# Optimization experiments

Hardware: AMD Instinct MI355X
Metric: run time of the kernel (lower is better)

## Reference

```python
import jax, jax.numpy as jnp
import numpy as np

N = 100000      # nodes per node type
E = 500000      # edges per relation
DIN = 128
DOUT = 128
H = 8
DK = DOUT // H  # 16
SQRT_DK = float(np.sqrt(DK))


def setup_inputs() -> dict:
    key = jax.random.key(0)
    ks = jax.random.split(key, 24)
    s = 1.0 / np.sqrt(DIN)
    inp = {
        "h_a": jax.random.normal(ks[0], (N, DIN), jnp.float32),
        "h_b": jax.random.normal(ks[1], (N, DIN), jnp.float32),
        "src0": jax.random.randint(ks[2], (E,), 0, N, jnp.int32),
        "dst0": jax.random.randint(ks[3], (E,), 0, N, jnp.int32),
        "src1": jax.random.randint(ks[4], (E,), 0, N, jnp.int32),
        "dst1": jax.random.randint(ks[5], (E,), 0, N, jnp.int32),
        "src2": jax.random.randint(ks[6], (E,), 0, N, jnp.int32),
        "dst2": jax.random.randint(ks[7], (E,), 0, N, jnp.int32),
        "Wk": jax.random.normal(ks[8], (2, DIN, DOUT), jnp.float32) * s,
        "bk": jnp.zeros((2, DOUT), jnp.float32),
        "Wv": jax.random.normal(ks[9], (2, DIN, DOUT), jnp.float32) * s,
        "bv": jnp.zeros((2, DOUT), jnp.float32),
        "Wq": jax.random.normal(ks[10], (2, DIN, DOUT), jnp.float32) * s,
        "bq": jnp.zeros((2, DOUT), jnp.float32),
        "Wa": jax.random.normal(ks[11], (2, DOUT, DOUT), jnp.float32) * s,
        "ba": jnp.zeros((2, DOUT), jnp.float32),
        # xavier_uniform-like scale for [H, DK, DK] relation transforms
        "rel_att": jax.random.normal(ks[12], (3, H, DK, DK), jnp.float32) * (1.0 / np.sqrt(DK)),
        "rel_msg": jax.random.normal(ks[13], (3, H, DK, DK), jnp.float32) * (1.0 / np.sqrt(DK)),
        "rel_pri": 1.0 + 0.1 * jax.random.normal(ks[14], (3, H), jnp.float32),
        "skip": jnp.zeros((2,), jnp.float32),
    }
    return inp


def _relation(x_src, x_dst, src, dst, Wk_, bk_, Wv_, bv_, Wq_, bq_, att, msg, pri):
    """One canonical edge type: returns scatter-sum aggregation t [N, H, DK]."""
    k = (x_src @ Wk_ + bk_).reshape(-1, H, DK)
    k = jnp.einsum('nhd,hde->nhe', k, att)                     # relation-specific key transform
    v = jnp.einsum('nhd,hde->nhe', (x_src @ Wv_ + bv_).reshape(-1, H, DK), msg)
    q = (x_dst @ Wq_ + bq_).reshape(-1, H, DK)
    # per-edge dot-product score [E, H] (v_dot_u with q on dst, k on src)
    score = jnp.einsum('ehd,ehd->eh', q[dst], k[src]) * pri / SQRT_DK
    # edge softmax grouped by dst node
    smax = jax.ops.segment_max(score, dst, num_segments=N)
    smax = jnp.where(jnp.isfinite(smax), smax, 0.0)            # empty dst groups
    ex = jnp.exp(score - smax[dst])
    den = jax.ops.segment_sum(ex, dst, num_segments=N)
    a = ex / den[dst]                                          # [E, H]
    # message = v[src] * a, scatter-sum to dst
    return jax.ops.segment_sum(v[src] * a[..., None], dst, num_segments=N)


def reference(h_a, h_b, src0, dst0, src1, dst1, src2, dst2,
              Wk, bk, Wv, bv, Wq, bq, Wa, ba,
              rel_att, rel_msg, rel_pri, skip):
    # relations: 0: a->b, 1: b->a, 2: a->b
    t0 = _relation(h_a, h_b, src0, dst0, Wk[0], bk[0], Wv[0], bv[0], Wq[1], bq[1],
                   rel_att[0], rel_msg[0], rel_pri[0])
    t1 = _relation(h_b, h_a, src1, dst1, Wk[1], bk[1], Wv[1], bv[1], Wq[0], bq[0],
                   rel_att[1], rel_msg[1], rel_pri[1])
    t2 = _relation(h_a, h_b, src2, dst2, Wk[0], bk[0], Wv[0], bv[0], Wq[1], bq[1],
                   rel_att[2], rel_msg[2], rel_pri[2])
    t_a = t1.reshape(N, DOUT)                  # cross_reducer mean over 1 relation
    t_b = ((t0 + t2) * 0.5).reshape(N, DOUT)   # mean over 2 relations into type b

    def node_out(t, h, i):
        alpha = jax.nn.sigmoid(skip[i])
        o = t @ Wa[i] + ba[i]                  # dropout = identity (eval)
        return o * alpha + h * (1.0 - alpha)

    out_a = node_out(t_a, h_a, 0)
    out_b = node_out(t_b, h_b, 1)
    return jnp.stack([out_a, out_b])           # [2, N, DOUT]
```

## Files before the change

kernel.cpp:

```cpp
#include <hip/hip_runtime.h>
#include <math.h>

typedef short bf16x8 __attribute__((ext_vector_type(8)));
typedef float f32x4 __attribute__((ext_vector_type(4)));
typedef float f32x2 __attribute__((ext_vector_type(2)));

__device__ __forceinline__ unsigned short cvt_bf16(float f) {
    unsigned u = __float_as_uint(f);
    u += 0x7fffu + ((u >> 16) & 1);
    return (unsigned short)(u >> 16);
}
__device__ __forceinline__ float cvt_f32(unsigned short b) {
    return __uint_as_float(((unsigned)b) << 16);
}
__device__ __forceinline__ f32x2 bf16pair(unsigned u) {
    f32x2 r;
    r.x = __uint_as_float(u << 16);
    r.y = __uint_as_float(u & 0xffff0000u);
    return r;
}

__global__ void compose_kernel(const float* __restrict__ Wk, const float* __restrict__ bk,
                               const float* __restrict__ Wv, const float* __restrict__ bv,
                               const float* __restrict__ att, const float* __restrict__ msg,
                               const float* __restrict__ pri,
                               unsigned short* __restrict__ WkT, unsigned short* __restrict__ WvT,
                               float* __restrict__ bkC, float* __restrict__ bvC) {
    int tid = blockIdx.x * blockDim.x + threadIdx.x;
    if (tid >= 3 * 16384) return;
    int r = tid / 16384;
    int rem = tid & 16383;
    int c = rem >> 7;
    int i = rem & 127;
    int h = c >> 4, e = c & 15;
    int wsel = (r == 1) ? 1 : 0;
    float p = pri[r * 8 + h] * 0.25f;

    const float* wkrow = Wk + wsel * 16384 + i * 128 + h * 16;
    const float* wvrow = Wv + wsel * 16384 + i * 128 + h * 16;
    const float* attc = att + ((r * 8 + h) * 16) * 16 + e;
    const float* msgc = msg + ((r * 8 + h) * 16) * 16 + e;
    float aK = 0.f, aV = 0.f;
#pragma unroll
    for (int d = 0; d < 16; ++d) {
        aK += wkrow[d] * attc[d * 16];
        aV += wvrow[d] * msgc[d * 16];
    }
    WkT[r * 16384 + c * 128 + i] = cvt_bf16(aK * p);
    WvT[r * 16384 + c * 128 + i] = cvt_bf16(aV);
    if (i == 0) {
        const float* bkr = bk + wsel * 128 + h * 16;
        const float* bvr = bv + wsel * 128 + h * 16;
        float bK = 0.f, bV = 0.f;
#pragma unroll
        for (int d = 0; d < 16; ++d) {
            bK += bkr[d] * attc[d * 16];
            bV += bvr[d] * msgc[d * 16];
        }
        bkC[r * 128 + c] = bK * p;
        bvC[r * 128 + c] = bV;
    }
}

__global__ void tcast4_kernel(const float* __restrict__ Wq, const float* __restrict__ Wa,
                              unsigned short* __restrict__ WqT, unsigned short* __restrict__ WaT) {
    int m = blockIdx.y;
    const float* src = (m < 2) ? Wq + m * 16384 : Wa + (m - 2) * 16384;
    unsigned short* dst = (m < 2) ? WqT + m * 16384 : WaT + (m - 2) * 16384;
    int tid = blockIdx.x * 256 + threadIdx.x;
    int c = tid >> 7, i = tid & 127;
    dst[tid] = cvt_bf16(src[i * 128 + c]);
}

__global__ void cast2_kernel(const float* __restrict__ a, const float* __restrict__ b,
                             unsigned short* __restrict__ da, unsigned short* __restrict__ db,
                             int n4) {
    int t = blockIdx.x * 256 + threadIdx.x;
    if (t >= 2 * n4) return;
    int sel = t >= n4;
    int i = sel ? t - n4 : t;
    const float* s = sel ? b : a;
    unsigned short* d = sel ? db : da;
    float4 f = ((const float4*)s)[i];
    ushort4 o;
    o.x = cvt_bf16(f.x); o.y = cvt_bf16(f.y); o.z = cvt_bf16(f.z); o.w = cvt_bf16(f.w);
    ((ushort4*)d)[i] = o;
}

struct OutSpec { const unsigned short* Wt; const float* bias; unsigned short* out; };
struct OutSpecs8 { OutSpec o[8]; };

#define LPAD 136

__global__ __launch_bounds__(256) void mfma_proj2_kernel(const unsigned short* __restrict__ Xa,
                                                         const unsigned short* __restrict__ Xb,
                                                         int nrows, OutSpecs8 specs, int gA) {
    __shared__ unsigned short Xs[128 * LPAD];
    __shared__ unsigned short Ws[128 * LPAD];
    __shared__ float bs[128];
    int tid = threadIdx.x;
    int aSide = blockIdx.x < gA;
    const unsigned short* X = aSide ? Xa : Xb;
    int obase = aSide ? 0 : 5;
    int nout = aSide ? 5 : 3;
    int n0 = (aSide ? blockIdx.x : blockIdx.x - gA) * 128;
    int rows_in = nrows - n0; if (rows_in > 128) rows_in = 128;

    {
        int rowb = tid >> 4, seg = tid & 15;
#pragma unroll
        for (int p = 0; p < 8; ++p) {
            int row = p * 16 + rowb;
            int rowg = row < rows_in ? row : rows_in - 1;
            uint4 d = *(const uint4*)(X + ((size_t)(n0 + rowg)) * 128 + seg * 8);
            *(uint4*)&Xs[row * LPAD + seg * 8] = d;
        }
    }

    int wave = tid >> 6, lane = tid & 63;
    int l15 = lane & 15, quad = lane >> 4;

    for (int oo = 0; oo < nout; ++oo) {
        const unsigned short* Wt = specs.o[obase + oo].Wt;
        const float* bias = specs.o[obase + oo].bias;
        unsigned short* out = specs.o[obase + oo].out;
        {
            int rowb = tid >> 4, seg = tid & 15;
#pragma unroll
            for (int p = 0; p < 8; ++p) {
                int row = p * 16 + rowb;
                uint4 d = *(const uint4*)(Wt + (size_t)row * 128 + seg * 8);
                *(uint4*)&Ws[row * LPAD + seg * 8] = d;
            }
            if (tid < 128) bs[tid] = bias[tid];
        }
        __syncthreads();

        f32x4 acc[2][8];
#pragma unroll
        for (int mi = 0; mi < 2; ++mi)
#pragma unroll
            for (int nt = 0; nt < 8; ++nt) acc[mi][nt] = (f32x4){0.f, 0.f, 0.f, 0.f};

#pragma unroll
        for (int ks = 0; ks < 4; ++ks) {
            bf16x8 afr[2];
            afr[0] = *(const bf16x8*)&Xs[(wave * 32 + l15) * LPAD + ks * 32 + quad * 8];
            afr[1] = *(const bf16x8*)&Xs[(wave * 32 + 16 + l15) * LPAD + ks * 32 + quad * 8];
#pragma unroll
            for (int nt = 0; nt < 8; ++nt) {
                bf16x8 bfr = *(const bf16x8*)&Ws[(nt * 16 + l15) * LPAD + ks * 32 + quad * 8];
                acc[0][nt] = __builtin_amdgcn_mfma_f32_16x16x32_bf16(afr[0], bfr, acc[0][nt], 0, 0, 0);
                acc[1][nt] = __builtin_amdgcn_mfma_f32_16x16x32_bf16(afr[1], bfr, acc[1][nt], 0, 0, 0);
            }
        }

#pragma unroll
        for (int mi = 0; mi < 2; ++mi) {
            int rowbase = wave * 32 + mi * 16 + quad * 4;
#pragma unroll
            for (int r = 0; r < 4; ++r) {
                int row = rowbase + r;
                if (row < rows_in) {
#pragma unroll
                    for (int nt = 0; nt < 8; ++nt) {
                        int col = nt * 16 + l15;
                        out[(size_t)(n0 + row) * 128 + col] = cvt_bf16(acc[mi][nt][r] + bs[col]);
                    }
                }
            }
        }
        __syncthreads();
    }
}

__global__ __launch_bounds__(256) void mfma_out2_kernel(
        const unsigned short* __restrict__ ta, const unsigned short* __restrict__ tb,
        const unsigned short* __restrict__ WaT, const float* __restrict__ ba,
        const float* __restrict__ h_a, const float* __restrict__ h_b,
        const float* __restrict__ skipv, float* __restrict__ outbase,
        int nrows, int gA) {
    __shared__ unsigned short Xs[128 * LPAD];
    __shared__ unsigned short Ws[128 * LPAD];
    __shared__ float bs[128];
    int tid = threadIdx.x;
    int sel = blockIdx.x >= gA;
    int n0 = (sel ? blockIdx.x - gA : blockIdx.x) * 128;
    const unsigned short* T16 = sel ? tb : ta;
    const unsigned short* W = WaT + sel * 16384;
    const float* bias = ba + sel * 128;
    const float* resid = sel ? h_b : h_a;
    float* out = outbase + (size_t)sel * nrows * 128;
    int rows_in = nrows - n0; if (rows_in > 128) rows_in = 128;

    {
        int rowb = tid >> 4, seg = tid & 15;
#pragma unroll
        for (int p = 0; p < 8; ++p) {
            int row = p * 16 + rowb;
            int rowg = row < rows_in ? row : rows_in - 1;
            uint4 d = *(const uint4*)(T16 + ((size_t)(n0 + rowg)) * 128 + seg * 8);
            *(uint4*)&Xs[row * LPAD + seg * 8] = d;
            uint4 w = *(const uint4*)(W + (size_t)row * 128 + seg * 8);
            *(uint4*)&Ws[row * LPAD + seg * 8] = w;
        }
        if (tid < 128) bs[tid] = bias[tid];
    }
    __syncthreads();

    int wave = tid >> 6, lane = tid & 63;
    int l15 = lane & 15, quad = lane >> 4;

    f32x4 acc[2][8];
#pragma unroll
    for (int mi = 0; mi < 2; ++mi)
#pragma unroll
        for (int nt = 0; nt < 8; ++nt) acc[mi][nt] = (f32x4){0.f, 0.f, 0.f, 0.f};

#pragma unroll
    for (int ks = 0; ks < 4; ++ks) {
        bf16x8 afr[2];
        afr[0] = *(const bf16x8*)&Xs[(wave * 32 + l15) * LPAD + ks * 32 + quad * 8];
        afr[1] = *(const bf16x8*)&Xs[(wave * 32 + 16 + l15) * LPAD + ks * 32 + quad * 8];
#pragma unroll
        for (int nt = 0; nt < 8; ++nt) {
            bf16x8 bfr = *(const bf16x8*)&Ws[(nt * 16 + l15) * LPAD + ks * 32 + quad * 8];
            acc[0][nt] = __builtin_amdgcn_mfma_f32_16x16x32_bf16(afr[0], bfr, acc[0][nt], 0, 0, 0);
            acc[1][nt] = __builtin_amdgcn_mfma_f32_16x16x32_bf16(afr[1], bfr, acc[1][nt], 0, 0, 0);
        }
    }

    float s = skipv[sel];
    float alpha = 1.f / (1.f + __expf(-s));
    float beta = 1.f - alpha;
#pragma unroll
    for (int mi = 0; mi < 2; ++mi) {
        int rowbase = wave * 32 + mi * 16 + quad * 4;
#pragma unroll
        for (int r = 0; r < 4; ++r) {
            int row = rowbase + r;
            if (row < rows_in) {
#pragma unroll
                for (int nt = 0; nt < 8; ++nt) {
                    int col = nt * 16 + l15;
                    size_t gi = (size_t)(n0 + row) * 128 + col;
                    out[gi] = alpha * (acc[mi][nt][r] + bs[col]) + beta * resid[gi];
                }
            }
        }
    }
}

__global__ void count3_kernel(const int* __restrict__ d0, const int* __restrict__ d1,
                              const int* __restrict__ d2, int* __restrict__ cnt3,
                              int E, int N) {
    int t = blockIdx.x * 256 + threadIdx.x;
    if (t >= 3 * E) return;
    int r = (t >= 2 * E) ? 2 : (t >= E ? 1 : 0);
    int e = t - r * E;
    const int* d = (r == 0) ? d0 : ((r == 1) ? d1 : d2);
    atomicAdd(&cnt3[r * N + d[e]], 1);
}

#define SCAN_B 256
__global__ void scan1_kernel(const int* __restrict__ cnt, int* __restrict__ offs,
                             int* __restrict__ bsum, int n) {
    __shared__ int sh[SCAN_B];
    int rbase = blockIdx.y * n;
    int i = blockIdx.x * SCAN_B + threadIdx.x;
    int v = (i < n) ? cnt[rbase + i] : 0;
    sh[threadIdx.x] = v;
    __syncthreads();
    for (int off = 1; off < SCAN_B; off <<= 1) {
        int t = (threadIdx.x >= off) ? sh[threadIdx.x - off] : 0;
        __syncthreads();
        sh[threadIdx.x] += t;
        __syncthreads();
    }
    if (i < n) offs[rbase + i] = sh[threadIdx.x] - v;
    if (threadIdx.x == SCAN_B - 1) bsum[blockIdx.y * 512 + blockIdx.x] = sh[threadIdx.x];
}

__global__ void scan2_kernel(int* __restrict__ bsum, int nb) {
    __shared__ int sh[512];
    int* bs = bsum + blockIdx.x * 512;
    int v = (threadIdx.x < nb) ? bs[threadIdx.x] : 0;
    sh[threadIdx.x] = v;
    __syncthreads();
    for (int off = 1; off < 512; off <<= 1) {
        int t = (threadIdx.x >= off) ? sh[threadIdx.x - off] : 0;
        __syncthreads();
        sh[threadIdx.x] += t;
        __syncthreads();
    }
    if (threadIdx.x < nb) bs[threadIdx.x] = sh[threadIdx.x] - v;
}

__global__ void scan3_kernel(int* __restrict__ offs, const int* __restrict__ bsum,
                             int* __restrict__ fill, int n) {
    int rbase = blockIdx.y * n;
    int i = blockIdx.x * SCAN_B + threadIdx.x;
    if (i < n) {
        int o = offs[rbase + i] + bsum[blockIdx.y * 512 + blockIdx.x];
        offs[rbase + i] = o;
        fill[rbase + i] = o;
    }
}

__global__ void scatter3_kernel(const int* __restrict__ s0, const int* __restrict__ d0,
                                const int* __restrict__ s1, const int* __restrict__ d1,
                                const int* __restrict__ s2, const int* __restrict__ d2,
                                int* __restrict__ fill3, int* __restrict__ ss3,
                                int E, int N) {
    int t = blockIdx.x * 256 + threadIdx.x;
    if (t >= 3 * E) return;
    int r = (t >= 2 * E) ? 2 : (t >= E ? 1 : 0);
    int e = t - r * E;
    const int* sp = (r == 0) ? s0 : ((r == 1) ? s1 : s2);
    const int* dp = (r == 0) ? d0 : ((r == 1) ? d1 : d2);
    int p = atomicAdd(&fill3[r * N + dp[e]], 1);
    ss3[(size_t)r * E + p] = sp[e];
}

struct AggSt { float den; f32x2 acc[8]; };

__device__ __forceinline__ void agg_loop(const unsigned short* __restrict__ k,
                                         const unsigned short* __restrict__ v,
                                         const int* __restrict__ ss,
                                         int start, int deg, int j, int h,
                                         const f32x2* q2, AggSt& st) {
    st.den = 0.f;
#pragma unroll
    for (int t = 0; t < 8; ++t) st.acc[t] = (f32x2){0.f, 0.f};
    for (int i = j; i < deg; i += 4) {
        int s = ss[start + i];
        const uint4* kp = (const uint4*)(k + (size_t)s * 128 + h * 16);
        uint4 ka = kp[0], kb = kp[1];
        const uint4* vp = (const uint4*)(v + (size_t)s * 128 + h * 16);
        uint4 va = vp[0], vb = vp[1];

        f32x2 d2 = (f32x2){0.f, 0.f};
        d2 += q2[0] * bf16pair(ka.x);
        d2 += q2[1] * bf16pair(ka.y);
        d2 += q2[2] * bf16pair(ka.z);
        d2 += q2[3] * bf16pair(ka.w);
        d2 += q2[4] * bf16pair(kb.x);
        d2 += q2[5] * bf16pair(kb.y);
        d2 += q2[6] * bf16pair(kb.z);
        d2 += q2[7] * bf16pair(kb.w);
        float sc = d2.x + d2.y;
        float ex = __expf(sc);
        st.den += ex;
        f32x2 exv = (f32x2){ex, ex};
        st.acc[0] += exv * bf16pair(va.x);
        st.acc[1] += exv * bf16pair(va.y);
        st.acc[2] += exv * bf16pair(va.z);
        st.acc[3] += exv * bf16pair(va.w);
        st.acc[4] += exv * bf16pair(vb.x);
        st.acc[5] += exv * bf16pair(vb.y);
        st.acc[6] += exv * bf16pair(vb.z);
        st.acc[7] += exv * bf16pair(vb.w);
    }
}

__device__ __forceinline__ void butterfly32(AggSt& st) {
#pragma unroll
    for (int mask = 8; mask <= 16; mask <<= 1) {
        st.den += __shfl_xor(st.den, mask);
#pragma unroll
        for (int t = 0; t < 8; ++t) {
            st.acc[t].x += __shfl_xor(st.acc[t].x, mask);
            st.acc[t].y += __shfl_xor(st.acc[t].y, mask);
        }
    }
}

__device__ __forceinline__ void load_q(const unsigned short* __restrict__ q,
                                       int wid, int h, f32x2* q2) {
    const uint4* qp = (const uint4*)(q + (size_t)wid * 128 + h * 16);
    uint4 qa = qp[0], qb = qp[1];
    q2[0] = bf16pair(qa.x); q2[1] = bf16pair(qa.y);
    q2[2] = bf16pair(qa.z); q2[3] = bf16pair(qa.w);
    q2[4] = bf16pair(qb.x); q2[5] = bf16pair(qb.y);
    q2[6] = bf16pair(qb.z); q2[7] = bf16pair(qb.w);
}

__device__ __forceinline__ void store_bf16(unsigned short* __restrict__ outp,
                                           size_t base, const float* o) {
    unsigned short* op = outp + base;
    ushort4 p0, p1, p2, p3;
    p0.x = cvt_bf16(o[0]);  p0.y = cvt_bf16(o[1]);  p0.z = cvt_bf16(o[2]);  p0.w = cvt_bf16(o[3]);
    p1.x = cvt_bf16(o[4]);  p1.y = cvt_bf16(o[5]);  p1.z = cvt_bf16(o[6]);  p1.w = cvt_bf16(o[7]);
    p2.x = cvt_bf16(o[8]);  p2.y = cvt_bf16(o[9]);  p2.z = cvt_bf16(o[10]); p2.w = cvt_bf16(o[11]);
    p3.x = cvt_bf16(o[12]); p3.y = cvt_bf16(o[13]); p3.z = cvt_bf16(o[14]); p3.w = cvt_bf16(o[15]);
    ((ushort4*)op)[0] = p0; ((ushort4*)op)[1] = p1;
    ((ushort4*)op)[2] = p2; ((ushort4*)op)[3] = p3;
}

__global__ __launch_bounds__(256) void agg_fused_kernel(
    const unsigned short* __restrict__ qb,
    const unsigned short* __restrict__ k0, const unsigned short* __restrict__ v0,
    const int* __restrict__ offs0, const int* __restrict__ cnt0, const int* __restrict__ ss0,
    const unsigned short* __restrict__ k2, const unsigned short* __restrict__ v2,
    const int* __restrict__ offs2, const int* __restrict__ cnt2, const int* __restrict__ ss2,
    const unsigned short* __restrict__ qa,
    const unsigned short* __restrict__ k1, const unsigned short* __restrict__ v1,
    const int* __restrict__ offs1, const int* __restrict__ cnt1, const int* __restrict__ ss1,
    unsigned short* __restrict__ tb16, unsigned short* __restrict__ ta16,
    int N, int bblk) {
    int bid = blockIdx.x;
    int l32 = threadIdx.x & 31;
    int j = l32 >> 3, h = l32 & 7;

    if (bid < bblk) {
        int wid = (bid * 256 + (int)threadIdx.x) >> 5;
        if (wid >= N) return;
        int start0 = offs0[wid], deg0 = cnt0[wid];
        int start2 = offs2[wid], deg2 = cnt2[wid];
        f32x2 q2[8];
        load_q(qb, wid, h, q2);

        AggSt s0, s2;
        agg_loop(k0, v0, ss0, start0, deg0, j, h, q2, s0);
        agg_loop(k2, v2, ss2, start2, deg2, j, h, q2, s2);
        butterfly32(s0);
        butterfly32(s2);

        if (j == 0) {
            float i0 = (deg0 > 0) ? (0.5f / s0.den) : 0.f;
            float i2 = (deg2 > 0) ? (0.5f / s2.den) : 0.f;
            float o[16];
#pragma unroll
            for (int t = 0; t < 8; ++t) {
                o[2 * t]     = s0.acc[t].x * i0 + s2.acc[t].x * i2;
                o[2 * t + 1] = s0.acc[t].y * i0 + s2.acc[t].y * i2;
            }
            store_bf16(tb16, (size_t)wid * 128 + h * 16, o);
        }
    } else {
        int wid = ((bid - bblk) * 256 + (int)threadIdx.x) >> 5;
        if (wid >= N) return;
        int start1 = offs1[wid], deg1 = cnt1[wid];
        f32x2 q2[8];
        load_q(qa, wid, h, q2);

        AggSt s1;
        agg_loop(k1, v1, ss1, start1, deg1, j, h, q2, s1);
        butterfly32(s1);

        if (j == 0) {
            float i1 = (deg1 > 0) ? (1.0f / s1.den) : 0.f;
            float o[16];
#pragma unroll
            for (int t = 0; t < 8; ++t) {
                o[2 * t]     = s1.acc[t].x * i1;
                o[2 * t + 1] = s1.acc[t].y * i1;
            }
            store_bf16(ta16, (size_t)wid * 128 + h * 16, o);
        }
    }
}

extern "C" void kernel_launch(void* const* d_in, const int* in_sizes, int n_in,
                              void* d_out, int out_size, void* d_ws, size_t ws_size,
                              hipStream_t stream) {
    const float* h_a = (const float*)d_in[0];
    const float* h_b = (const float*)d_in[1];
    const int* srcs[3] = {(const int*)d_in[2], (const int*)d_in[4], (const int*)d_in[6]};
    const int* dsts[3] = {(const int*)d_in[3], (const int*)d_in[5], (const int*)d_in[7]};
    const float* Wk = (const float*)d_in[8];
    const float* bk = (const float*)d_in[9];
    const float* Wv = (const float*)d_in[10];
    const float* bv = (const float*)d_in[11];
    const float* Wq = (const float*)d_in[12];
    const float* bq = (const float*)d_in[13];
    const float* Wa = (const float*)d_in[14];
    const float* ba = (const float*)d_in[15];
    const float* att = (const float*)d_in[16];
    const float* msg = (const float*)d_in[17];
    const float* pri = (const float*)d_in[18];
    const float* skip = (const float*)d_in[19];

    const int N = in_sizes[0] / 128;
    const int E = in_sizes[2];
    const size_t NC = (size_t)N * 128;

    char* P = (char*)d_ws;
    auto alloc = [&](size_t bytes) { char* p = P; P += (bytes + 255) & ~(size_t)255; return p; };

    unsigned short* WkT = (unsigned short*)alloc(3 * 16384 * 2);
    unsigned short* WvT = (unsigned short*)alloc(3 * 16384 * 2);
    unsigned short* WqT = (unsigned short*)alloc(2 * 16384 * 2);
    unsigned short* WaT = (unsigned short*)alloc(2 * 16384 * 2);
    float* bkC = (float*)alloc(3 * 128 * 4);
    float* bvC = (float*)alloc(3 * 128 * 4);
    unsigned short* Xa16 = (unsigned short*)alloc(NC * 2);
    unsigned short* Xb16 = (unsigned short*)alloc(NC * 2);
    unsigned short* qa16 = (unsigned short*)alloc(NC * 2);
    unsigned short* qb16 = (unsigned short*)alloc(NC * 2);
    unsigned short* k16[3], *v16[3];
    for (int r = 0; r < 3; ++r) {
        k16[r] = (unsigned short*)alloc(NC * 2);
        v16[r] = (unsigned short*)alloc(NC * 2);
    }
    unsigned short* ta16 = (unsigned short*)alloc(NC * 2);
    unsigned short* tb16 = (unsigned short*)alloc(NC * 2);
    int* cnt3 = (int*)alloc((size_t)3 * N * 4);
    int* offs3 = (int*)alloc((size_t)3 * N * 4);
    int* fill3 = (int*)alloc((size_t)3 * N * 4);
    int* ss3 = (int*)alloc((size_t)3 * E * 4);
    int* bsum = (int*)alloc(3 * 512 * 4);

    int eb3 = (3 * E + 255) / 256;
    int scanb = (N + SCAN_B - 1) / SCAN_B;

    hipMemsetAsync(cnt3, 0, (size_t)3 * N * sizeof(int), stream);
    count3_kernel<<<eb3, 256, 0, stream>>>(dsts[0], dsts[1], dsts[2], cnt3, E, N);
    scan1_kernel<<<dim3(scanb, 3), SCAN_B, 0, stream>>>(cnt3, offs3, bsum, N);
    scan2_kernel<<<3, 512, 0, stream>>>(bsum, scanb);
    scan3_kernel<<<dim3(scanb, 3), SCAN_B, 0, stream>>>(offs3, bsum, fill3, N);
    scatter3_kernel<<<eb3, 256, 0, stream>>>(srcs[0], dsts[0], srcs[1], dsts[1],
                                             srcs[2], dsts[2], fill3, ss3, E, N);

    compose_kernel<<<(3 * 16384 + 255) / 256, 256, 0, stream>>>(
        Wk, bk, Wv, bv, att, msg, pri, WkT, WvT, bkC, bvC);
    tcast4_kernel<<<dim3(64, 4), 256, 0, stream>>>(Wq, Wa, WqT, WaT);

    int n4 = (int)(NC / 4);
    cast2_kernel<<<(2 * n4 + 255) / 256, 256, 0, stream>>>(h_a, h_b, Xa16, Xb16, n4);

    int gblocks = (N + 127) / 128;

    OutSpecs8 s8;
    s8.o[0] = {WqT, bq, qa16};
    s8.o[1] = {WkT + 0 * 16384, bkC + 0 * 128, k16[0]};
    s8.o[2] = {WvT + 0 * 16384, bvC + 0 * 128, v16[0]};
    s8.o[3] = {WkT + 2 * 16384, bkC + 2 * 128, k16[2]};
    s8.o[4] = {WvT + 2 * 16384, bvC + 2 * 128, v16[2]};
    s8.o[5] = {WqT + 16384, bq + 128, qb16};
    s8.o[6] = {WkT + 1 * 16384, bkC + 1 * 128, k16[1]};
    s8.o[7] = {WvT + 1 * 16384, bvC + 1 * 128, v16[1]};
    mfma_proj2_kernel<<<2 * gblocks, 256, 0, stream>>>(Xa16, Xb16, N, s8, gblocks);

    int bblk = (N + 7) / 8;
    agg_fused_kernel<<<2 * bblk, 256, 0, stream>>>(
        qb16, k16[0], v16[0], offs3 + 0 * N, cnt3 + 0 * N, ss3 + 0 * (size_t)E,
        k16[2], v16[2], offs3 + 2 * N, cnt3 + 2 * N, ss3 + 2 * (size_t)E,
        qa16, k16[1], v16[1], offs3 + 1 * N, cnt3 + 1 * N, ss3 + 1 * (size_t)E,
        tb16, ta16, N, bblk);

    mfma_out2_kernel<<<2 * gblocks, 256, 0, stream>>>(
        ta16, tb16, WaT, ba, h_a, h_b, skip, (float*)d_out, N, gblocks);
}
```

Baseline: 654.4 us.

## Fuse input bf16 cast into projection and interleave gather loops in aggregation

Removes the standalone cast kernel. The projection kernel now reads the fp32 node features directly and converts them to bf16 while staging into shared memory, which avoids writing and re-reading the bf16 copies. The aggregation kernel interleaves its two relation gather loops in one loop on the b side and processes two edges per iteration on the a side, so more independent gathers are in flight. It also interleaves a-side and b-side blocks by blockIdx parity for better balance. Costs are higher register pressure and predicated dummy loads of row 0 when degrees differ.

```diff
diff --git a/kernel.cpp b/kernel.cpp
--- a/kernel.cpp
+++ b/kernel.cpp
@@ -72,35 +72,20 @@
     dst[tid] = cvt_bf16(src[i * 128 + c]);
 }
 
-__global__ void cast2_kernel(const float* __restrict__ a, const float* __restrict__ b,
-                             unsigned short* __restrict__ da, unsigned short* __restrict__ db,
-                             int n4) {
-    int t = blockIdx.x * 256 + threadIdx.x;
-    if (t >= 2 * n4) return;
-    int sel = t >= n4;
-    int i = sel ? t - n4 : t;
-    const float* s = sel ? b : a;
-    unsigned short* d = sel ? db : da;
-    float4 f = ((const float4*)s)[i];
-    ushort4 o;
-    o.x = cvt_bf16(f.x); o.y = cvt_bf16(f.y); o.z = cvt_bf16(f.z); o.w = cvt_bf16(f.w);
-    ((ushort4*)d)[i] = o;
-}
-
 struct OutSpec { const unsigned short* Wt; const float* bias; unsigned short* out; };
 struct OutSpecs8 { OutSpec o[8]; };
 
 #define LPAD 136
 
-__global__ __launch_bounds__(256) void mfma_proj2_kernel(const unsigned short* __restrict__ Xa,
-                                                         const unsigned short* __restrict__ Xb,
+__global__ __launch_bounds__(256) void mfma_proj2_kernel(const float* __restrict__ Xa,
+                                                         const float* __restrict__ Xb,
                                                          int nrows, OutSpecs8 specs, int gA) {
     __shared__ unsigned short Xs[128 * LPAD];
     __shared__ unsigned short Ws[128 * LPAD];
     __shared__ float bs[128];
     int tid = threadIdx.x;
     int aSide = blockIdx.x < gA;
-    const unsigned short* X = aSide ? Xa : Xb;
+    const float* X = aSide ? Xa : Xb;
     int obase = aSide ? 0 : 5;
     int nout = aSide ? 5 : 3;
     int n0 = (aSide ? blockIdx.x : blockIdx.x - gA) * 128;
@@ -112,8 +97,14 @@
         for (int p = 0; p < 8; ++p) {
             int row = p * 16 + rowb;
             int rowg = row < rows_in ? row : rows_in - 1;
-            uint4 d = *(const uint4*)(X + ((size_t)(n0 + rowg)) * 128 + seg * 8);
-            *(uint4*)&Xs[row * LPAD + seg * 8] = d;
+            const float* src = X + ((size_t)(n0 + rowg)) * 128 + seg * 8;
+            float4 f0 = ((const float4*)src)[0];
+            float4 f1 = ((const float4*)src)[1];
+            ushort4 o0, o1;
+            o0.x = cvt_bf16(f0.x); o0.y = cvt_bf16(f0.y); o0.z = cvt_bf16(f0.z); o0.w = cvt_bf16(f0.w);
+            o1.x = cvt_bf16(f1.x); o1.y = cvt_bf16(f1.y); o1.z = cvt_bf16(f1.z); o1.w = cvt_bf16(f1.w);
+            *(ushort4*)&Xs[row * LPAD + seg * 8] = o0;
+            *(ushort4*)&Xs[row * LPAD + seg * 8 + 4] = o1;
         }
     }
 
@@ -322,59 +313,6 @@
     ss3[(size_t)r * E + p] = sp[e];
 }
 
-struct AggSt { float den; f32x2 acc[8]; };
-
-__device__ __forceinline__ void agg_loop(const unsigned short* __restrict__ k,
-                                         const unsigned short* __restrict__ v,
-                                         const int* __restrict__ ss,
-                                         int start, int deg, int j, int h,
-                                         const f32x2* q2, AggSt& st) {
-    st.den = 0.f;
-#pragma unroll
-    for (int t = 0; t < 8; ++t) st.acc[t] = (f32x2){0.f, 0.f};
-    for (int i = j; i < deg; i += 4) {
-        int s = ss[start + i];
-        const uint4* kp = (const uint4*)(k + (size_t)s * 128 + h * 16);
-        uint4 ka = kp[0], kb = kp[1];
-        const uint4* vp = (const uint4*)(v + (size_t)s * 128 + h * 16);
-        uint4 va = vp[0], vb = vp[1];
-
-        f32x2 d2 = (f32x2){0.f, 0.f};
-        d2 += q2[0] * bf16pair(ka.x);
-        d2 += q2[1] * bf16pair(ka.y);
-        d2 += q2[2] * bf16pair(ka.z);
-        d2 += q2[3] * bf16pair(ka.w);
-        d2 += q2[4] * bf16pair(kb.x);
-        d2 += q2[5] * bf16pair(kb.y);
-        d2 += q2[6] * bf16pair(kb.z);
-        d2 += q2[7] * bf16pair(kb.w);
-        float sc = d2.x + d2.y;
-        float ex = __expf(sc);
-        st.den += ex;
-        f32x2 exv = (f32x2){ex, ex};
-        st.acc[0] += exv * bf16pair(va.x);
-        st.acc[1] += exv * bf16pair(va.y);
-        st.acc[2] += exv * bf16pair(va.z);
-        st.acc[3] += exv * bf16pair(va.w);
-        st.acc[4] += exv * bf16pair(vb.x);
-        st.acc[5] += exv * bf16pair(vb.y);
-        st.acc[6] += exv * bf16pair(vb.z);
-        st.acc[7] += exv * bf16pair(vb.w);
-    }
-}
-
-__device__ __forceinline__ void butterfly32(AggSt& st) {
-#pragma unroll
-    for (int mask = 8; mask <= 16; mask <<= 1) {
-        st.den += __shfl_xor(st.den, mask);
-#pragma unroll
-        for (int t = 0; t < 8; ++t) {
-            st.acc[t].x += __shfl_xor(st.acc[t].x, mask);
-            st.acc[t].y += __shfl_xor(st.acc[t].y, mask);
-        }
-    }
-}
-
 __device__ __forceinline__ void load_q(const unsigned short* __restrict__ q,
                                        int wid, int h, f32x2* q2) {
     const uint4* qp = (const uint4*)(q + (size_t)wid * 128 + h * 16);
@@ -397,6 +335,20 @@
     ((ushort4*)op)[2] = p2; ((ushort4*)op)[3] = p3;
 }
 
+#define DOT8(d, q2, A, B) \
+    d = (f32x2){0.f, 0.f}; \
+    d += q2[0] * bf16pair(A.x); d += q2[1] * bf16pair(A.y); \
+    d += q2[2] * bf16pair(A.z); d += q2[3] * bf16pair(A.w); \
+    d += q2[4] * bf16pair(B.x); d += q2[5] * bf16pair(B.y); \
+    d += q2[6] * bf16pair(B.z); d += q2[7] * bf16pair(B.w);
+
+#define ACC8(acc, ex, A, B) { \
+    f32x2 _e = (f32x2){ex, ex}; \
+    acc[0] += _e * bf16pair(A.x); acc[1] += _e * bf16pair(A.y); \
+    acc[2] += _e * bf16pair(A.z); acc[3] += _e * bf16pair(A.w); \
+    acc[4] += _e * bf16pair(B.x); acc[5] += _e * bf16pair(B.y); \
+    acc[6] += _e * bf16pair(B.z); acc[7] += _e * bf16pair(B.w); }
+
 __global__ __launch_bounds__(256) void agg_fused_kernel(
     const unsigned short* __restrict__ qb,
     const unsigned short* __restrict__ k0, const unsigned short* __restrict__ v0,
@@ -407,54 +359,121 @@
     const unsigned short* __restrict__ k1, const unsigned short* __restrict__ v1,
     const int* __restrict__ offs1, const int* __restrict__ cnt1, const int* __restrict__ ss1,
     unsigned short* __restrict__ tb16, unsigned short* __restrict__ ta16,
-    int N, int bblk) {
-    int bid = blockIdx.x;
+    int N) {
+    int side = blockIdx.x & 1;
+    int bidx = blockIdx.x >> 1;
     int l32 = threadIdx.x & 31;
     int j = l32 >> 3, h = l32 & 7;
-
-    if (bid < bblk) {
-        int wid = (bid * 256 + (int)threadIdx.x) >> 5;
-        if (wid >= N) return;
+    int wid = (bidx * 256 + (int)threadIdx.x) >> 5;
+    if (wid >= N) return;
+
+    if (side == 0) {
         int start0 = offs0[wid], deg0 = cnt0[wid];
         int start2 = offs2[wid], deg2 = cnt2[wid];
         f32x2 q2[8];
         load_q(qb, wid, h, q2);
 
-        AggSt s0, s2;
-        agg_loop(k0, v0, ss0, start0, deg0, j, h, q2, s0);
-        agg_loop(k2, v2, ss2, start2, deg2, j, h, q2, s2);
-        butterfly32(s0);
-        butterfly32(s2);
+        float den0 = 0.f, den2 = 0.f;
+        f32x2 a0[8], a2[8];
+#pragma unroll
+        for (int t = 0; t < 8; ++t) { a0[t] = (f32x2){0.f, 0.f}; a2[t] = (f32x2){0.f, 0.f}; }
+
+        int i0 = j, i2 = j;
+        while ((i0 < deg0) || (i2 < deg2)) {
+            bool c0 = i0 < deg0, c2 = i2 < deg2;
+            int s0 = c0 ? ss0[start0 + i0] : 0;
+            int s2 = c2 ? ss2[start2 + i2] : 0;
+            const uint4* k0p = (const uint4*)(k0 + (size_t)s0 * 128 + h * 16);
+            const uint4* v0p = (const uint4*)(v0 + (size_t)s0 * 128 + h * 16);
+            const uint4* k2p = (const uint4*)(k2 + (size_t)s2 * 128 + h * 16);
+            const uint4* v2p = (const uint4*)(v2 + (size_t)s2 * 128 + h * 16);
+            uint4 kA0 = k0p[0], kB0 = k0p[1], vA0 = v0p[0], vB0 = v0p[1];
+            uint4 kA2 = k2p[0], kB2 = k2p[1], vA2 = v2p[0], vB2 = v2p[1];
+
+            f32x2 d0, d2v;
+            DOT8(d0, q2, kA0, kB0);
+            DOT8(d2v, q2, kA2, kB2);
+            float ex0 = c0 ? __expf(d0.x + d0.y) : 0.f;
+            float ex2 = c2 ? __expf(d2v.x + d2v.y) : 0.f;
+            den0 += ex0; den2 += ex2;
+            ACC8(a0, ex0, vA0, vB0);
+            ACC8(a2, ex2, vA2, vB2);
+            i0 += 4; i2 += 4;
+        }
+
+#pragma unroll
+        for (int mask = 8; mask <= 16; mask <<= 1) {
+            den0 += __shfl_xor(den0, mask);
+            den2 += __shfl_xor(den2, mask);
+#pragma unroll
+            for (int t = 0; t < 8; ++t) {
+                a0[t].x += __shfl_xor(a0[t].x, mask);
+                a0[t].y += __shfl_xor(a0[t].y, mask);
+                a2[t].x += __shfl_xor(a2[t].x, mask);
+                a2[t].y += __shfl_xor(a2[t].y, mask);
+            }
+        }
 
         if (j == 0) {
-            float i0 = (deg0 > 0) ? (0.5f / s0.den) : 0.f;
-            float i2 = (deg2 > 0) ? (0.5f / s2.den) : 0.f;
+            float i0s = (deg0 > 0) ? (0.5f / den0) : 0.f;
+            float i2s = (deg2 > 0) ? (0.5f / den2) : 0.f;
             float o[16];
 #pragma unroll
             for (int t = 0; t < 8; ++t) {
-                o[2 * t]     = s0.acc[t].x * i0 + s2.acc[t].x * i2;
-                o[2 * t + 1] = s0.acc[t].y * i0 + s2.acc[t].y * i2;
+                o[2 * t]     = a0[t].x * i0s + a2[t].x * i2s;
+                o[2 * t + 1] = a0[t].y * i0s + a2[t].y * i2s;
             }
             store_bf16(tb16, (size_t)wid * 128 + h * 16, o);
         }
     } else {
-        int wid = ((bid - bblk) * 256 + (int)threadIdx.x) >> 5;
-        if (wid >= N) return;
         int start1 = offs1[wid], deg1 = cnt1[wid];
         f32x2 q2[8];
         load_q(qa, wid, h, q2);
 
-        AggSt s1;
-        agg_loop(k1, v1, ss1, start1, deg1, j, h, q2, s1);
-        butterfly32(s1);
+        float den = 0.f;
+        f32x2 ac[8];
+#pragma unroll
+        for (int t = 0; t < 8; ++t) ac[t] = (f32x2){0.f, 0.f};
+
+        for (int i = j; i < deg1; i += 8) {
+            int iB = i + 4;
+            bool cB = iB < deg1;
+            int sA = ss1[start1 + i];
+            int sB = cB ? ss1[start1 + iB] : 0;
+            const uint4* kAp = (const uint4*)(k1 + (size_t)sA * 128 + h * 16);
+            const uint4* vAp = (const uint4*)(v1 + (size_t)sA * 128 + h * 16);
+            const uint4* kBp = (const uint4*)(k1 + (size_t)sB * 128 + h * 16);
+            const uint4* vBp = (const uint4*)(v1 + (size_t)sB * 128 + h * 16);
+            uint4 kAa = kAp[0], kAb = kAp[1], vAa = vAp[0], vAb = vAp[1];
+            uint4 kBa = kBp[0], kBb = kBp[1], vBa = vBp[0], vBb = vBp[1];
+
+            f32x2 dA, dB;
+            DOT8(dA, q2, kAa, kAb);
+            DOT8(dB, q2, kBa, kBb);
+            float exA = __expf(dA.x + dA.y);
+            float exB = cB ? __expf(dB.x + dB.y) : 0.f;
+            den += exA + exB;
+            ACC8(ac, exA, vAa, vAb);
+            ACC8(ac, exB, vBa, vBb);
+        }
+
+#pragma unroll
+        for (int mask = 8; mask <= 16; mask <<= 1) {
+            den += __shfl_xor(den, mask);
+#pragma unroll
+            for (int t = 0; t < 8; ++t) {
+                ac[t].x += __shfl_xor(ac[t].x, mask);
+                ac[t].y += __shfl_xor(ac[t].y, mask);
+            }
+        }
 
         if (j == 0) {
-            float i1 = (deg1 > 0) ? (1.0f / s1.den) : 0.f;
+            float inv = (deg1 > 0) ? (1.0f / den) : 0.f;
             float o[16];
 #pragma unroll
             for (int t = 0; t < 8; ++t) {
-                o[2 * t]     = s1.acc[t].x * i1;
-                o[2 * t + 1] = s1.acc[t].y * i1;
+                o[2 * t]     = ac[t].x * inv;
+                o[2 * t + 1] = ac[t].y * inv;
             }
             store_bf16(ta16, (size_t)wid * 128 + h * 16, o);
         }
@@ -494,8 +513,6 @@
     unsigned short* WaT = (unsigned short*)alloc(2 * 16384 * 2);
     float* bkC = (float*)alloc(3 * 128 * 4);
     float* bvC = (float*)alloc(3 * 128 * 4);
-    unsigned short* Xa16 = (unsigned short*)alloc(NC * 2);
-    unsigned short* Xb16 = (unsigned short*)alloc(NC * 2);
     unsigned short* qa16 = (unsigned short*)alloc(NC * 2);
     unsigned short* qb16 = (unsigned short*)alloc(NC * 2);
     unsigned short* k16[3], *v16[3];
@@ -525,9 +542,6 @@
     compose_kernel<<<(3 * 16384 + 255) / 256, 256, 0, stream>>>(
         Wk, bk, Wv, bv, att, msg, pri, WkT, WvT, bkC, bvC);
     tcast4_kernel<<<dim3(64, 4), 256, 0, stream>>>(Wq, Wa, WqT, WaT);
-
-    int n4 = (int)(NC / 4);
-    cast2_kernel<<<(2 * n4 + 255) / 256, 256, 0, stream>>>(h_a, h_b, Xa16, Xb16, n4);
 
     int gblocks = (N + 127) / 128;
 
@@ -540,14 +554,14 @@
     s8.o[5] = {WqT + 16384, bq + 128, qb16};
     s8.o[6] = {WkT + 1 * 16384, bkC + 1 * 128, k16[1]};
     s8.o[7] = {WvT + 1 * 16384, bvC + 1 * 128, v16[1]};
-    mfma_proj2_kernel<<<2 * gblocks, 256, 0, stream>>>(Xa16, Xb16, N, s8, gblocks);
+    mfma_proj2_kernel<<<2 * gblocks, 256, 0, stream>>>(h_a, h_b, N, s8, gblocks);
 
     int bblk = (N + 7) / 8;
     agg_fused_kernel<<<2 * bblk, 256, 0, stream>>>(
         qb16, k16[0], v16[0], offs3 + 0 * N, cnt3 + 0 * N, ss3 + 0 * (size_t)E,
         k16[2], v16[2], offs3 + 2 * N, cnt3 + 2 * N, ss3 + 2 * (size_t)E,
         qa16, k16[1], v16[1], offs3 + 1 * N, cnt3 + 1 * N, ss3 + 1 * (size_t)E,
-        tb16, ta16, N, bblk);
+        tb16, ta16, N);
 
     mfma_out2_kernel<<<2 * gblocks, 256, 0, stream>>>(
         ta16, tb16, WaT, ba, h_a, h_b, skip, (float*)d_out, N, gblocks);
```

Measured after the change: 684.8 us. 4.6% more time.
